# Performance work log

Hardware: AMD Instinct MI355X
Metric: run time of the kernel (lower is better)

Reference implementation:

```python
import jax, jax.numpy as jnp
import numpy as np

NUM = 5          # spline intervals
KS = 3           # spline order k
GRID_LO, GRID_HI = -1.0, 1.0
KH = KW = 3      # kernel size
STRIDE = 1
PAD = 1
DIL = 1


def make_grid():
    # extended uniform grid: num+2k+1 points from lo-k*h to hi+k*h (h=(hi-lo)/num)
    h = (GRID_HI - GRID_LO) / NUM
    return GRID_LO + jnp.arange(-KS, NUM + KS + 1, dtype=jnp.float32) * h  # (12,)


def b_spline_basis(x, grid, k):
    # x: (..., ), grid: (G,) shared across features (all rows of pykan grid identical)
    # returns (..., G-1-k) Cox-de Boor bases of order k
    x = x[..., None]
    B = ((x >= grid[:-1]) & (x < grid[1:])).astype(x.dtype)
    for p in range(1, k + 1):
        left = (x - grid[:-(p + 1)]) / (grid[p:-1] - grid[:-(p + 1)]) * B[..., :-1]
        right = (grid[p + 1:] - x) / (grid[p + 1:] - grid[1:-p]) * B[..., 1:]
        B = left + right
    return B


def extract_patches(x):
    # torch.nn.Unfold ordering: (B, C, kh*kw, OH, OW), kernel positions row-major
    x = jnp.pad(x, ((0, 0), (0, 0), (PAD, PAD), (PAD, PAD)))
    B, C, H, W = x.shape
    OH = (H - DIL * (KH - 1) - 1) // STRIDE + 1
    OW = (W - DIL * (KW - 1) - 1) // STRIDE + 1
    pats = []
    for i in range(KH):
        for j in range(KW):
            pats.append(x[:, :, i * DIL:i * DIL + STRIDE * (OH - 1) + 1:STRIDE,
                          j * DIL:j * DIL + STRIDE * (OW - 1) + 1:STRIDE])
    return jnp.stack(pats, axis=2)  # (B, C, K, OH, OW)


def setup_inputs() -> dict:
    key = jax.random.key(0)
    k1, k2, k3, k4, k5 = jax.random.split(key, 5)
    B, C, O, H, W = 8, 32, 64, 32, 32
    K, M = KH * KW, NUM + KS
    x = jax.random.normal(k1, (B, C, H, W), dtype=jnp.float32)
    coef = jax.random.normal(k2, (O, C, K, M), dtype=jnp.float32) * 0.1
    scale_base = jax.random.normal(k3, (O, C, K), dtype=jnp.float32) / np.sqrt(K)
    scale_sp = jnp.ones((O, C, K), dtype=jnp.float32)
    bias = jnp.zeros((O,), dtype=jnp.float32)
    return {"x": x, "coef": coef, "scale_base": scale_base,
            "scale_sp": scale_sp, "bias": bias}


def reference(x, coef, scale_base, scale_sp, bias):
    grid = make_grid()
    p = extract_patches(x)                              # (B, C, K, OH, OW)
    B, C, K, OH, OW = p.shape
    t = p.transpose(0, 1, 3, 4, 2).reshape(B, C, OH * OW, K)  # (B, C, L, K)
    Bsp = b_spline_basis(t, grid, KS)                   # (B, C, L, K, M)
    silu = t * jax.nn.sigmoid(t)
    W_sp = scale_sp[..., None] * coef                   # (O, C, K, M)
    out = (jnp.einsum('bclk,ock->bol', silu, scale_base)
           + jnp.einsum('bclkm,ockm->bol', Bsp, W_sp))
    out = out + bias[None, :, None]
    return out.reshape(B, -1, OH, OW)
```

## Files before the change

kernel.cpp:

```cpp
#include <hip/hip_runtime.h>


typedef __attribute__((ext_vector_type(8))) short v8s;
typedef __attribute__((ext_vector_type(4))) float v4f;
typedef unsigned short ushort_t;

#define WB_ELEMS    (64u * 2592u)
#define CELL_STRIDE 296
#define ROW_STRIDE  (34 * CELL_STRIDE)

__device__ __forceinline__ unsigned short f2bf(float v) {
  union { float f; unsigned int u; } w; w.f = v;
  unsigned int r = w.u + 0x7FFFu + ((w.u >> 16) & 1u);
  return (unsigned short)(r >> 16);
}

__global__ __launch_bounds__(256) void kan_prep(const float* __restrict__ coef,
                                                const float* __restrict__ sb,
                                                const float* __restrict__ ssp,
                                                ushort_t* __restrict__ Wb) {
  int i = blockIdx.x * 256 + threadIdx.x;
  if (i >= (int)WB_ELEMS) return;
  int o = i / 2592;
  int r = i - o * 2592;
  int pos = r / 288;
  int rj = r - pos * 288;
  int j = rj >> 5;
  int c = rj & 31;
  int sidx = (o * 32 + c) * 9 + pos;
  float val = (j == 0) ? sb[sidx] : ssp[sidx] * coef[sidx * 8 + (j - 1)];
  Wb[i] = f2bf(val);
}

template <int LO, int HI>
__device__ __forceinline__ void kloop(const ushort_t* __restrict__ fb,
                                      const ushort_t* __restrict__ wp,
                                      v4f& acc0, v4f& acc1) {
#pragma unroll
  for (int s = LO; s < HI; ++s) {
    const int di = s / 27;
    const int dj = (s / 9) % 3;
    const int kk = s % 9;
    const int fo = di * ROW_STRIDE + dj * CELL_STRIDE + kk * 32;
    v8s wf = *(const v8s*)(wp + s * 32);
    v8s a0 = *(const v8s*)(fb + fo);
    v8s a1 = *(const v8s*)(fb + fo + 16 * CELL_STRIDE);
    acc0 = __builtin_amdgcn_mfma_f32_16x16x32_bf16(wf, a0, acc0, 0, 0, 0);
    acc1 = __builtin_amdgcn_mfma_f32_16x16x32_bf16(wf, a1, acc1, 0, 0, 0);
  }
}

__global__ __launch_bounds__(512, 4) void kan_fused(const float* __restrict__ x,
                                                    const ushort_t* __restrict__ Wb,
                                                    const float* __restrict__ bias,
                                                    float* __restrict__ out) {
  __shared__ ushort_t feat[3 * ROW_STRIDE];
  __shared__ float xs[32 * 33];

  const int tid = threadIdx.x;
  const int bx = blockIdx.x;
  const int ohalf = bx & 1;
  const int oh = (bx >> 1) & 31;
  const int b = bx >> 6;

  for (int r = 0; r < 3; ++r) {
    const int h = oh + r - 1;
    const bool hval = (h >= 0) && (h < 32);
    if (hval) {
      int idx = tid * 2;
      int c = idx >> 5, w = idx & 31;
      float2 v = *(const float2*)(x + (((b * 32 + c) * 32 + h) * 32 + w));
      xs[c * 33 + w] = v.x;
      xs[c * 33 + w + 1] = v.y;
    }
    __syncthreads();
    for (int idx = tid; idx < 1088; idx += 512) {
      int c = idx & 31, cell = idx >> 5;
      int wi = cell - 1;
      float t = 0.0f;
      if (hval && wi >= 0 && wi < 32) t = xs[c * 33 + wi];

      unsigned short f0 = f2bf(t / (1.0f + __expf(-t)));
      float u  = (t + 2.2f) * 2.5f;
      float fi = floorf(u);
      int   i  = (int)fi;
      float s  = u - fi;
      float s2 = s * s, s3 = s2 * s;
      float om = 1.0f - s;
      float w0 = om * om * om * (1.0f / 6.0f);
      float w1 = (4.0f - 6.0f * s2 + 3.0f * s3) * (1.0f / 6.0f);
      float w2 = (1.0f + 3.0f * s + 3.0f * s2 - 3.0f * s3) * (1.0f / 6.0f);
      float w3 = s3 * (1.0f / 6.0f);

      ushort_t* dst = feat + r * ROW_STRIDE + cell * CELL_STRIDE + c;
      dst[0] = f0;
#pragma unroll
      for (int jj = 0; jj < 8; ++jj) {
        int d = jj - i + 3;
        float bv = (d == 0) ? w0 : (d == 1) ? w1 : (d == 2) ? w2 : (d == 3) ? w3 : 0.0f;
        dst[(jj + 1) * 32] = f2bf(bv);
      }
    }
    __syncthreads();
  }

  const int wv   = tid >> 6;
  const int lane = tid & 63;
  const int row  = lane & 15;
  const int quad = lane >> 4;
  const int og   = wv & 1;
  const int kq   = wv >> 1;
  const int obase = ohalf * 32 + og * 16;

  const ushort_t* fb = feat + row * CELL_STRIDE + quad * 8;
  const ushort_t* wp = Wb + (size_t)(obase + row) * 2592 + quad * 8;

  v4f acc0 = {0.f, 0.f, 0.f, 0.f};
  v4f acc1 = acc0;

  if (kq == 0)      kloop<0, 20>(fb, wp, acc0, acc1);
  else if (kq == 1) kloop<20, 40>(fb, wp, acc0, acc1);
  else if (kq == 2) kloop<40, 60>(fb, wp, acc0, acc1);
  else              kloop<60, 81>(fb, wp, acc0, acc1);

  __syncthreads();
  float* red = (float*)feat;
  if (kq != 0) {
    float* rp = red + ((kq - 1) * 2 + og) * 512 + quad * 4 * 32 + row;
#pragma unroll
    for (int r = 0; r < 4; ++r) {
      rp[r * 32]      = acc0[r];
      rp[r * 32 + 16] = acc1[r];
    }
  }
  __syncthreads();
  if (kq == 0) {
    float* o0 = out + ((size_t)(b * 64 + obase + quad * 4)) * 1024 + oh * 32 + row;
#pragma unroll
    for (int r = 0; r < 4; ++r) {
      float bv = bias[obase + quad * 4 + r];
      float s0 = acc0[r], s1 = acc1[r];
#pragma unroll
      for (int gs = 0; gs < 3; ++gs) {
        const float* rp = red + (gs * 2 + og) * 512 + (quad * 4 + r) * 32 + row;
        s0 += rp[0];
        s1 += rp[16];
      }
      o0[(size_t)r * 1024]      = s0 + bv;
      o0[(size_t)r * 1024 + 16] = s1 + bv;
    }
  }
}

extern "C" void kernel_launch(void* const* d_in, const int* in_sizes, int n_in,
                              void* d_out, int out_size, void* d_ws, size_t ws_size,
                              hipStream_t stream) {
  const float* x    = (const float*)d_in[0];
  const float* coef = (const float*)d_in[1];
  const float* sb   = (const float*)d_in[2];
  const float* ssp  = (const float*)d_in[3];
  const float* bias = (const float*)d_in[4];
  float* out = (float*)d_out;

  ushort_t* Wb = (ushort_t*)d_ws;

  hipLaunchKernelGGL(kan_prep, dim3(648), dim3(256), 0, stream, coef, sb, ssp, Wb);
  hipLaunchKernelGGL(kan_fused, dim3(512), dim3(512), 0, stream, x, Wb, bias, out);
}
```

Baseline: 83.67 us.

## Load all three input rows at once and pack feature writes into 16-byte LDS stores

```diff
diff --git a/kernel.cpp b/kernel.cpp
--- a/kernel.cpp
+++ b/kernel.cpp
@@ -55,7 +55,7 @@
                                                     const float* __restrict__ bias,
                                                     float* __restrict__ out) {
   __shared__ ushort_t feat[3 * ROW_STRIDE];
-  __shared__ float xs[32 * 33];
+  __shared__ float xs[3][32][33];
 
   const int tid = threadIdx.x;
   const int bx = blockIdx.x;
@@ -63,27 +63,42 @@
   const int oh = (bx >> 1) & 31;
   const int b = bx >> 6;
 
-  for (int r = 0; r < 3; ++r) {
-    const int h = oh + r - 1;
-    const bool hval = (h >= 0) && (h < 32);
-    if (hval) {
-      int idx = tid * 2;
-      int c = idx >> 5, w = idx & 31;
-      float2 v = *(const float2*)(x + (((b * 32 + c) * 32 + h) * 32 + w));
-      xs[c * 33 + w] = v.x;
-      xs[c * 33 + w + 1] = v.y;
+  {
+    int idx = tid * 2;
+    int c = idx >> 5, w = idx & 31;
+    const float* xpc = x + ((b * 32 + c) * 32) * 32 + w;
+#pragma unroll
+    for (int r = 0; r < 3; ++r) {
+      int h = oh + r - 1;
+      if (h >= 0 && h < 32) {
+        float2 v = *(const float2*)(xpc + h * 32);
+        xs[r][c][w] = v.x;
+        xs[r][c][w + 1] = v.y;
+      }
     }
-    __syncthreads();
-    for (int idx = tid; idx < 1088; idx += 512) {
-      int c = idx & 31, cell = idx >> 5;
-      int wi = cell - 1;
-      float t = 0.0f;
-      if (hval && wi >= 0 && wi < 32) t = xs[c * 33 + wi];
+  }
+  __syncthreads();
 
-      unsigned short f0 = f2bf(t / (1.0f + __expf(-t)));
+  if (tid < 408) {
+    int r = tid / 136;
+    int rem = tid - r * 136;
+    int cell = rem >> 2;
+    int cg = rem & 3;
+    int c0 = cg * 8;
+    int h = oh + r - 1;
+    int wi = cell - 1;
+    bool tval = (h >= 0) && (h < 32) && (wi >= 0) && (wi < 32);
+
+    unsigned int pk[9][4];
+#pragma unroll
+    for (int i = 0; i < 8; ++i) {
+      float t = tval ? xs[r][c0 + i][wi] : 0.0f;
+
+      unsigned short us[9];
+      us[0] = f2bf(t / (1.0f + __expf(-t)));
       float u  = (t + 2.2f) * 2.5f;
       float fi = floorf(u);
-      int   i  = (int)fi;
+      int   iu = (int)fi;
       float s  = u - fi;
       float s2 = s * s, s3 = s2 * s;
       float om = 1.0f - s;
@@ -91,18 +106,27 @@
       float w1 = (4.0f - 6.0f * s2 + 3.0f * s3) * (1.0f / 6.0f);
       float w2 = (1.0f + 3.0f * s + 3.0f * s2 - 3.0f * s3) * (1.0f / 6.0f);
       float w3 = s3 * (1.0f / 6.0f);
-
-      ushort_t* dst = feat + r * ROW_STRIDE + cell * CELL_STRIDE + c;
-      dst[0] = f0;
 #pragma unroll
       for (int jj = 0; jj < 8; ++jj) {
-        int d = jj - i + 3;
+        int d = jj - iu + 3;
         float bv = (d == 0) ? w0 : (d == 1) ? w1 : (d == 2) ? w2 : (d == 3) ? w3 : 0.0f;
-        dst[(jj + 1) * 32] = f2bf(bv);
+        us[jj + 1] = f2bf(bv);
+      }
+#pragma unroll
+      for (int j = 0; j < 9; ++j) {
+        unsigned int half = (unsigned int)us[j];
+        if (i & 1) pk[j][i >> 1] |= half << 16;
+        else       pk[j][i >> 1]  = half;
       }
     }
-    __syncthreads();
+
+    ushort_t* dstc = feat + r * ROW_STRIDE + cell * CELL_STRIDE + c0;
+#pragma unroll
+    for (int j = 0; j < 9; ++j) {
+      *(uint4*)(dstc + j * 32) = make_uint4(pk[j][0], pk[j][1], pk[j][2], pk[j][3]);
+    }
   }
+  __syncthreads();
 
   const int wv   = tid >> 6;
   const int lane = tid & 63;
```

After: 85.28 us. Within noise of the previous version (+1.9%).
